# Optimization experiments

Hardware: AMD Instinct MI355X
Metric: run time of the kernel (lower is better)

Reference implementation:

```python
import jax, jax.numpy as jnp
import numpy as np

NUM_OPS = 8
NUM_CMP = 6
H = 2048
N = NUM_CMP + 2  # max number of anchors
NEG = -1e9


def setup_inputs() -> dict:
    key = jax.random.key(0)
    ks = jax.random.split(key, 8)
    s = 0.02
    return {
        "emb": jax.random.normal(ks[0], (NUM_OPS + 1, H), jnp.float32) * s,
        "w_ih": jax.random.normal(ks[1], (4 * H, H), jnp.float32) * s,
        "w_hh": jax.random.normal(ks[2], (4 * H, H), jnp.float32) * s,
        "b_ih": jnp.zeros((4 * H,), jnp.float32),
        "b_hh": jnp.zeros((4 * H,), jnp.float32),
        "w_opt": jax.random.normal(ks[3], (NUM_OPS, H), jnp.float32) * s,
        "b_opt": jnp.zeros((NUM_OPS,), jnp.float32),
        "w_attn1": jax.random.normal(ks[4], (H, H), jnp.float32) * s,
        "w_attn2": jax.random.normal(ks[5], (H, H), jnp.float32) * s,
        "v_attn": jax.random.normal(ks[6], (H,), jnp.float32) * s,
        "seed": 0,
    }


def _lstm(w_ih, w_hh, b_ih, b_hh, x, h, c):
    # torch LSTMCell, gate order i, f, g, o; x,h,c: [1,H]
    g = x @ w_ih.T + b_ih + h @ w_hh.T + b_hh
    i, f, gg, o = jnp.split(g, 4, axis=-1)
    c = jax.nn.sigmoid(f) * c + jax.nn.sigmoid(i) * jnp.tanh(gg)
    h = jax.nn.sigmoid(o) * jnp.tanh(c)
    return h, c


def _cat_stats(logits, idx):
    # cross_entropy(logits[None], idx) and detached entropy, logits: [K]
    logp = jax.nn.log_softmax(logits)
    lp = -logp[idx]
    logp_d = jax.lax.stop_gradient(logp)
    p = jnp.exp(logp_d)
    ent = -jnp.sum(jnp.where(p > 0, p * logp_d, 0.0))
    return lp, ent


def _generate_cell(params, hc, key):
    emb, w_ih, w_hh, b_ih, b_hh, w_opt, b_opt, w1, w2, v = params
    x = emb[0][None]  # [1,H]
    if hc is None:
        h = jnp.zeros((1, H), emb.dtype)
        c = jnp.zeros((1, H), emb.dtype)
    else:
        h, c = hc
    anchors = jnp.zeros((N, H), emb.dtype)
    anchors_w1 = jnp.zeros((N, H), emb.dtype)
    # two warmup steps; anchors stay zeros_like(h), anchors_w1 gets w1(h)
    for s in range(2):
        h, c = _lstm(w_ih, w_hh, b_ih, b_hh, x, h, c)
        anchors_w1 = anchors_w1.at[s].set((h @ w1.T)[0])

    def node_step(carry, inp):
        x, h, c, anchors, anchors_w1, ent, lp = carry
        s, k = inp
        mask = jnp.arange(N) < s
        idxs = []
        for i in range(2):
            h, c = _lstm(w_ih, w_hh, b_ih, b_hh, x, h, c)
            scores = jnp.tanh(h @ w2.T + anchors_w1) @ v  # [N]
            logits = jnp.where(mask, scores, NEG)
            idx = jax.random.categorical(jax.random.fold_in(k, i), logits)
            l, e = _cat_stats(logits, idx)
            lp = lp + l
            ent = ent + e
            x = anchors[idx][None]
            idxs.append(idx)
        ops = []
        for i in range(2):
            h, c = _lstm(w_ih, w_hh, b_ih, b_hh, x, h, c)
            logits = (h @ w_opt.T + b_opt)[0]  # [num_ops]
            op = jax.random.categorical(jax.random.fold_in(k, 2 + i), logits)
            l, e = _cat_stats(logits, op)
            lp = lp + l
            ent = ent + e
            x = emb[op + 1][None]
            ops.append(op)
        h, c = _lstm(w_ih, w_hh, b_ih, b_hh, x, h, c)
        anchors = anchors.at[s].set(h[0])
        anchors_w1 = anchors_w1.at[s].set((h @ w1.T)[0])
        x = emb[0][None]
        return (x, h, c, anchors, anchors_w1, ent, lp), (jnp.stack(idxs), jnp.stack(ops))

    zero = jnp.asarray(0.0, emb.dtype)
    carry0 = (x, h, c, anchors, anchors_w1, zero, zero)
    xs = (jnp.arange(2, N), jax.random.split(key, NUM_CMP))
    (x, h, c, _, _, ent, lp), (idx_seq, opt_seq) = jax.lax.scan(node_step, carry0, xs)
    return idx_seq, opt_seq, ent, lp, (h, c)


def reference(emb, w_ih, w_hh, b_ih, b_hh, w_opt, b_opt, w_attn1, w_attn2, v_attn, seed):
    params = (emb, w_ih, w_hh, b_ih, b_hh, w_opt, b_opt, w_attn1, w_attn2, v_attn)
    key = jax.random.key(seed)
    k1, k2 = jax.random.split(key)
    idx_n, opt_n, ent_n, lp_n, hc = _generate_cell(params, None, k1)
    idx_r, opt_r, ent_r, lp_r, _ = _generate_cell(params, hc, k2)
    return idx_n, opt_n, idx_r, opt_r, ent_n + ent_r, lp_n + lp_r
```

## Files before the change

kernel.cpp:

```cpp
#include <hip/hip_runtime.h>
#include <stdint.h>


#define HDIM 2048
#define NCAT 8
#define PARTITIONABLE 1

__device__ __forceinline__ unsigned rotl32(unsigned v, int r){ return (v<<r)|(v>>(32-r)); }

__device__ inline void tf_block(unsigned k0, unsigned k1, unsigned x0, unsigned x1,
                                unsigned& o0, unsigned& o1){
  unsigned ks0=k0, ks1=k1, ks2=0x1BD11BDAu ^ k0 ^ k1;
  const int ra[4]={13,15,26,6};
  const int rb[4]={17,29,16,24};
  x0 += ks0; x1 += ks1;
  #pragma unroll
  for (int i=0;i<4;++i){ x0+=x1; x1=rotl32(x1,ra[i]); x1^=x0; }
  x0+=ks1; x1+=ks2+1u;
  #pragma unroll
  for (int i=0;i<4;++i){ x0+=x1; x1=rotl32(x1,rb[i]); x1^=x0; }
  x0+=ks2; x1+=ks0+2u;
  #pragma unroll
  for (int i=0;i<4;++i){ x0+=x1; x1=rotl32(x1,ra[i]); x1^=x0; }
  x0+=ks0; x1+=ks1+3u;
  #pragma unroll
  for (int i=0;i<4;++i){ x0+=x1; x1=rotl32(x1,rb[i]); x1^=x0; }
  x0+=ks1; x1+=ks2+4u;
  #pragma unroll
  for (int i=0;i<4;++i){ x0+=x1; x1=rotl32(x1,ra[i]); x1^=x0; }
  x0+=ks2; x1+=ks0+5u;
  o0=x0; o1=x1;
}

__device__ __forceinline__ float sigm(float z){ return 1.0f/(1.0f+expf(-z)); }

__device__ inline int sample_and_stats(const float* logits, unsigned k0, unsigned k1,
                                       float* scal ){
  unsigned bits[NCAT];
#if PARTITIONABLE
  #pragma unroll
  for (int i=0;i<NCAT;++i){ unsigned a,b; tf_block(k0,k1,0u,(unsigned)i,a,b); bits[i]=a^b; }
#else
  #pragma unroll
  for (int i=0;i<4;++i){ unsigned a,b; tf_block(k0,k1,(unsigned)i,(unsigned)(i+4),a,b); bits[i]=a; bits[i+4]=b; }
#endif
  const float tiny = 1.1754943508222875e-38f;
  int best=0; float bv=-3.4e38f;
  #pragma unroll
  for (int j=0;j<NCAT;++j){
    float f = __uint_as_float((bits[j]>>9)|0x3f800000u) - 1.0f;
    float u = fmaxf(tiny, f*(1.0f-tiny)+tiny);
    float g = -logf(-logf(u));
    float vv = g + logits[j];
    if (vv > bv){ bv=vv; best=j; }
  }
  float m=-3.4e38f;
  #pragma unroll
  for (int j=0;j<NCAT;++j) m = fmaxf(m, logits[j]);
  float se=0.f;
  #pragma unroll
  for (int j=0;j<NCAT;++j) se += expf(logits[j]-m);
  float lse = logf(se);
  scal[1] += (m + lse - logits[best]);
  float ent = 0.f;
  #pragma unroll
  for (int j=0;j<NCAT;++j){
    float lpj = logits[j]-m-lse;
    float p = expf(lpj);
    if (p > 0.f) ent -= p*lpj;
  }
  scal[0] += ent;
  return best;
}


__global__ __launch_bounds__(256) void k_init(float* ws, const float* __restrict__ emb,
                                              const int* __restrict__ seedp, int cell){
  int t = threadIdx.x;
  float* anch = ws + 10240;
  float* aw1  = ws + 26624;
  for (int i=t;i<NCAT*HDIM;i+=256){ anch[i]=0.f; aw1[i]=0.f; }
  float* x = ws + 6144;
  for (int i=t;i<HDIM;i+=256){
    x[i] = emb[i];
    if (cell==0){ ws[i]=0.f; ws[4096+i]=0.f; }
  }
  if (t==0 && cell==0){
    float* scal = ws + 43008; scal[0]=0.f; scal[1]=0.f;
    unsigned* nk = (unsigned*)(ws + 43012);
    unsigned seed = (unsigned)seedp[0];
    unsigned K0=0u, K1=seed;
    unsigned ck[2][2];
#if PARTITIONABLE
    tf_block(K0,K1,0u,0u,ck[0][0],ck[0][1]);
    tf_block(K0,K1,0u,1u,ck[1][0],ck[1][1]);
    for (int cc=0;cc<2;++cc)
      for (int i=0;i<6;++i)
        tf_block(ck[cc][0],ck[cc][1],0u,(unsigned)i, nk[(cc*6+i)*2], nk[(cc*6+i)*2+1]);
#else
    unsigned a0,a1,b0,b1;
    tf_block(K0,K1,0u,2u,a0,a1);
    tf_block(K0,K1,1u,3u,b0,b1);
    ck[0][0]=a0; ck[0][1]=b0; ck[1][0]=a1; ck[1][1]=b1;
    for (int cc=0;cc<2;++cc){
      unsigned y0[6], y1[6];
      for (int i=0;i<6;++i) tf_block(ck[cc][0],ck[cc][1],(unsigned)i,(unsigned)(i+6),y0[i],y1[i]);
      unsigned flat[12];
      for (int i=0;i<6;++i){ flat[i]=y0[i]; flat[6+i]=y1[i]; }
      for (int i=0;i<6;++i){ nk[(cc*6+i)*2]=flat[2*i]; nk[(cc*6+i)*2+1]=flat[2*i+1]; }
    }
#endif
  }
}

__global__ __launch_bounds__(256) void k_lstm(
    const float* __restrict__ w_ih, const float* __restrict__ w_hh,
    const float* __restrict__ b_ih, const float* __restrict__ b_hh,
    const float* __restrict__ x, const float* __restrict__ h_in,
    float* __restrict__ h_out, float* __restrict__ c)
{
  int b  = blockIdx.x;
  int k0 = b*4;
  int wv = threadIdx.x >> 6;
  int ln = threadIdx.x & 63;
  __shared__ float gl[4][4];
  const float4* x4 = (const float4*)x;
  const float4* h4 = (const float4*)h_in;
  float acc[4];
  #pragma unroll
  for (int rr=0; rr<4; ++rr){
    int row = wv*HDIM + k0 + rr;
    const float4* wi = (const float4*)(w_ih + (size_t)row*HDIM);
    const float4* wh = (const float4*)(w_hh + (size_t)row*HDIM);
    float s = 0.f;
    #pragma unroll
    for (int it=0; it<8; ++it){
      int i4 = ln + it*64;
      float4 a = wi[i4]; float4 xv = x4[i4];
      float4 bb = wh[i4]; float4 hv = h4[i4];
      s += a.x*xv.x + a.y*xv.y + a.z*xv.z + a.w*xv.w;
      s += bb.x*hv.x + bb.y*hv.y + bb.z*hv.z + bb.w*hv.w;
    }
    acc[rr] = s;
  }
  #pragma unroll
  for (int rr=0; rr<4; ++rr){
    float s = acc[rr];
    #pragma unroll
    for (int m=32; m; m>>=1) s += __shfl_xor(s, m, 64);
    if (ln==0) gl[wv][rr] = s;
  }
  __syncthreads();
  if (threadIdx.x < 4){
    int kk = k0 + threadIdx.x;
    float gi = gl[0][threadIdx.x] + b_ih[kk]          + b_hh[kk];
    float gf = gl[1][threadIdx.x] + b_ih[HDIM+kk]     + b_hh[HDIM+kk];
    float gg = gl[2][threadIdx.x] + b_ih[2*HDIM+kk]   + b_hh[2*HDIM+kk];
    float go = gl[3][threadIdx.x] + b_ih[3*HDIM+kk]   + b_hh[3*HDIM+kk];
    float cn = sigm(gf)*c[kk] + sigm(gi)*tanhf(gg);
    c[kk] = cn;
    h_out[kk] = sigm(go)*tanhf(cn);
  }
}

__global__ __launch_bounds__(256) void k_matvec(const float* __restrict__ M,
    const float* __restrict__ vin, float* __restrict__ vout,
    const float* __restrict__ csrc, float* __restrict__ cdst,
    const float* __restrict__ xsrc, float* __restrict__ xdst)
{
  int b = blockIdx.x;
  int wv = threadIdx.x>>6, ln = threadIdx.x&63;
  const float4* v4 = (const float4*)vin;
  #pragma unroll
  for (int rr=0; rr<2; ++rr){
    int row = b*8 + wv*2 + rr;
    const float4* m4 = (const float4*)(M + (size_t)row*HDIM);
    float s=0.f;
    #pragma unroll
    for (int it=0; it<8; ++it){
      int i4 = ln + it*64;
      float4 a = m4[i4]; float4 v = v4[i4];
      s += a.x*v.x + a.y*v.y + a.z*v.z + a.w*v.w;
    }
    #pragma unroll
    for (int m=32; m; m>>=1) s += __shfl_xor(s, m, 64);
    if (ln==0) vout[row] = s;
  }
  int t = threadIdx.x;
  if (t < 8){
    int i = b*8 + t;
    if (cdst) cdst[i] = csrc[i];
    if (xdst) xdst[i] = xsrc[i];
  }
}

__global__ __launch_bounds__(512) void k_attn_sample(const float* __restrict__ t2,
    const float* __restrict__ aw1, const float* __restrict__ vatt,
    const float* __restrict__ anch, float* __restrict__ x, float* scal,
    const unsigned* __restrict__ nk, int cell, int node, int isub,
    float* __restrict__ outslot)
{
  __shared__ float sc[NCAT];
  __shared__ int sidx;
  int wv = threadIdx.x>>6, ln = threadIdx.x&63;
  const float* a = aw1 + (size_t)wv*HDIM;
  float s=0.f;
  for (int it=0; it<32; ++it){
    int d = ln + it*64;
    s += tanhf(t2[d] + a[d]) * vatt[d];
  }
  #pragma unroll
  for (int m=32; m; m>>=1) s += __shfl_xor(s, m, 64);
  if (ln==0) sc[wv]=s;
  __syncthreads();
  if (threadIdx.x==0){
    int svis = node + 2;
    float logits[NCAT];
    #pragma unroll
    for (int j=0;j<NCAT;++j) logits[j] = (j<svis)? sc[j] : -1e9f;
    unsigned f0,f1;
    tf_block(nk[(cell*6+node)*2], nk[(cell*6+node)*2+1], 0u, (unsigned)isub, f0, f1);
    int idx = sample_and_stats(logits, f0, f1, scal);
    *outslot = (float)idx;
    sidx = idx;
  }
  __syncthreads();
  const float* src = anch + (size_t)sidx*HDIM;
  for (int d=threadIdx.x; d<HDIM; d+=512) x[d]=src[d];
}

__global__ __launch_bounds__(512) void k_opt_sample(const float* __restrict__ h,
    const float* __restrict__ wopt, const float* __restrict__ bopt,
    const float* __restrict__ emb, float* __restrict__ x, float* scal,
    const unsigned* __restrict__ nk, int cell, int node, int isub,
    float* __restrict__ outslot)
{
  __shared__ float sc[NCAT];
  __shared__ int sop;
  int wv = threadIdx.x>>6, ln = threadIdx.x&63;
  const float4* m4 = (const float4*)(wopt + (size_t)wv*HDIM);
  const float4* h4 = (const float4*)h;
  float s=0.f;
  #pragma unroll
  for (int it=0; it<8; ++it){
    int i4 = ln + it*64;
    float4 a = m4[i4]; float4 v = h4[i4];
    s += a.x*v.x + a.y*v.y + a.z*v.z + a.w*v.w;
  }
  #pragma unroll
  for (int m=32; m; m>>=1) s += __shfl_xor(s, m, 64);
  if (ln==0) sc[wv] = s + bopt[wv];
  __syncthreads();
  if (threadIdx.x==0){
    float logits[NCAT];
    #pragma unroll
    for (int j=0;j<NCAT;++j) logits[j]=sc[j];
    unsigned f0,f1;
    tf_block(nk[(cell*6+node)*2], nk[(cell*6+node)*2+1], 0u, (unsigned)(2+isub), f0, f1);
    int op = sample_and_stats(logits, f0, f1, scal);
    *outslot = (float)op;
    sop = op;
  }
  __syncthreads();
  const float* src = emb + (size_t)(sop+1)*HDIM;
  for (int d=threadIdx.x; d<HDIM; d+=512) x[d]=src[d];
}

__global__ void k_fin(const float* __restrict__ scal, float* __restrict__ out){
  out[48] = scal[0];
  out[49] = scal[1];
}

extern "C" void kernel_launch(void* const* d_in, const int* in_sizes, int n_in,
                              void* d_out, int out_size, void* d_ws, size_t ws_size,
                              hipStream_t stream)
{
  (void)in_sizes; (void)n_in; (void)out_size; (void)ws_size;
  const float* emb   = (const float*)d_in[0];
  const float* w_ih  = (const float*)d_in[1];
  const float* w_hh  = (const float*)d_in[2];
  const float* b_ih  = (const float*)d_in[3];
  const float* b_hh  = (const float*)d_in[4];
  const float* w_opt = (const float*)d_in[5];
  const float* b_opt = (const float*)d_in[6];
  const float* w1    = (const float*)d_in[7];
  const float* w2    = (const float*)d_in[8];
  const float* vatt  = (const float*)d_in[9];
  const int*   seed  = (const int*)d_in[10];

  float* ws  = (float*)d_ws;
  float* out = (float*)d_out;

  float* h[2] = { ws+0, ws+2048 };
  float* c    = ws+4096;
  float* x    = ws+6144;
  float* t2   = ws+8192;
  float* anch = ws+10240;
  float* aw1  = ws+26624;
  float* scal = ws+43008;
  const unsigned* nk = (const unsigned*)(ws+43012);

  int cur = 0;
  for (int cell=0; cell<2; ++cell){
    k_init<<<1,256,0,stream>>>(ws, emb, seed, cell);
    for (int s=0; s<2; ++s){
      k_lstm<<<512,256,0,stream>>>(w_ih,w_hh,b_ih,b_hh,x,h[cur],h[cur^1],c); cur^=1;
      k_matvec<<<256,256,0,stream>>>(w1, h[cur], aw1 + s*HDIM,
                                     nullptr,nullptr,nullptr,nullptr);
    }
    for (int node=0; node<6; ++node){
      for (int i=0;i<2;++i){
        k_lstm<<<512,256,0,stream>>>(w_ih,w_hh,b_ih,b_hh,x,h[cur],h[cur^1],c); cur^=1;
        k_matvec<<<256,256,0,stream>>>(w2, h[cur], t2, nullptr,nullptr,nullptr,nullptr);
        k_attn_sample<<<1,512,0,stream>>>(t2, aw1, vatt, anch, x, scal, nk, cell, node, i,
                                          out + cell*24 + node*2 + i);
      }
      for (int i=0;i<2;++i){
        k_lstm<<<512,256,0,stream>>>(w_ih,w_hh,b_ih,b_hh,x,h[cur],h[cur^1],c); cur^=1;
        k_opt_sample<<<1,512,0,stream>>>(h[cur], w_opt, b_opt, emb, x, scal, nk, cell, node, i,
                                         out + cell*24 + 12 + node*2 + i);
      }
      k_lstm<<<512,256,0,stream>>>(w_ih,w_hh,b_ih,b_hh,x,h[cur],h[cur^1],c); cur^=1;
      k_matvec<<<256,256,0,stream>>>(w1, h[cur], aw1 + (node+2)*HDIM,
                                     h[cur], anch + (node+2)*HDIM, emb, x);
    }
  }
  k_fin<<<1,1,0,stream>>>(scal, out);
}
```

Before: 2.397 ms.

## Precompute embedding input gates, skip zero-input matvec, fuse sampling via last-block counters

Precomputes w_ih·emb[j]+bias for all nine embeddings so LSTM steps with embedding inputs skip the w_ih matvec, and skips it entirely when the input is a zero anchor. The input is tracked through a small control word rather than copied. Attention scoring and option sampling are folded into the preceding matvec kernels with an atomic last-block pattern, removing separate single-block launches. Each LSTM launch now runs more blocks with one row per block, at the cost of workspace for the gate table and atomic counters.

```diff
diff --git a/kernel.cpp b/kernel.cpp
--- a/kernel.cpp
+++ b/kernel.cpp
@@ -4,7 +4,22 @@
 
 #define HDIM 2048
 #define NCAT 8
+#define NROWS 8192
 #define PARTITIONABLE 1
+
+#define WS_H0    0
+#define WS_H1    2048
+#define WS_C     4096
+#define WS_X     6144
+#define WS_T2    8192
+#define WS_ANCH  10240
+#define WS_AW1   26624
+#define WS_SCAL  43008
+#define WS_XCTL  43010
+#define WS_NK    43012
+#define WS_CTR   43072
+#define WS_BIAS  43264
+#define WS_GIE   51456
 
 __device__ __forceinline__ unsigned rotl32(unsigned v, int r){ return (v<<r)|(v>>(32-r)); }
 
@@ -73,21 +88,53 @@
   return best;
 }
 
-
-__global__ __launch_bounds__(256) void k_init(float* ws, const float* __restrict__ emb,
-                                              const int* __restrict__ seedp, int cell){
+__global__ __launch_bounds__(256) void k_pre(const float* __restrict__ w_ih,
+    const float* __restrict__ b_ih, const float* __restrict__ b_hh,
+    const float* __restrict__ emb, float* __restrict__ gie, float* __restrict__ bias)
+{
+  int wv = threadIdx.x>>6, ln = threadIdx.x&63;
+  int r = blockIdx.x*4 + wv;
+  const float4* wr = (const float4*)(w_ih + (size_t)r*HDIM);
+  const float4* e4 = (const float4*)emb;
+  float acc[9];
+  #pragma unroll
+  for (int j=0;j<9;++j) acc[j]=0.f;
+  for (int it=0; it<8; ++it){
+    float4 a = wr[ln+it*64];
+    #pragma unroll
+    for (int j=0;j<9;++j){
+      float4 e = e4[j*512 + ln + it*64];
+      acc[j] += a.x*e.x + a.y*e.y + a.z*e.z + a.w*e.w;
+    }
+  }
+  #pragma unroll
+  for (int j=0;j<9;++j){
+    float s = acc[j];
+    #pragma unroll
+    for (int m=32;m;m>>=1) s += __shfl_xor(s,m,64);
+    acc[j]=s;
+  }
+  if (ln==0){
+    float b = b_ih[r] + b_hh[r];
+    bias[r] = b;
+    #pragma unroll
+    for (int j=0;j<9;++j) gie[(size_t)j*NROWS + r] = acc[j] + b;
+  }
+}
+
+__global__ __launch_bounds__(256) void k_init(float* ws, const int* __restrict__ seedp, int cell){
   int t = threadIdx.x;
-  float* anch = ws + 10240;
-  float* aw1  = ws + 26624;
+  float* anch = ws + WS_ANCH;
+  float* aw1  = ws + WS_AW1;
   for (int i=t;i<NCAT*HDIM;i+=256){ anch[i]=0.f; aw1[i]=0.f; }
-  float* x = ws + 6144;
-  for (int i=t;i<HDIM;i+=256){
-    x[i] = emb[i];
-    if (cell==0){ ws[i]=0.f; ws[4096+i]=0.f; }
-  }
+  if (cell==0){
+    for (int i=t;i<HDIM;i+=256){ ws[WS_H0+i]=0.f; ws[WS_C+i]=0.f; }
+    for (int i=t;i<64;i+=256) ((int*)(ws+WS_CTR))[i]=0;
+  }
+  if (t<2) ((int*)(ws+WS_XCTL))[t] = 0;
   if (t==0 && cell==0){
-    float* scal = ws + 43008; scal[0]=0.f; scal[1]=0.f;
-    unsigned* nk = (unsigned*)(ws + 43012);
+    ws[WS_SCAL]=0.f; ws[WS_SCAL+1]=0.f;
+    unsigned* nk = (unsigned*)(ws + WS_NK);
     unsigned seed = (unsigned)seedp[0];
     unsigned K0=0u, K1=seed;
     unsigned ck[2][2];
@@ -115,155 +162,185 @@
 
 __global__ __launch_bounds__(256) void k_lstm(
     const float* __restrict__ w_ih, const float* __restrict__ w_hh,
-    const float* __restrict__ b_ih, const float* __restrict__ b_hh,
-    const float* __restrict__ x, const float* __restrict__ h_in,
-    float* __restrict__ h_out, float* __restrict__ c)
+    const float* __restrict__ bias, const float* __restrict__ gie,
+    const int* __restrict__ xctl, const float* __restrict__ x,
+    const float* __restrict__ h_in, float* __restrict__ h_out, float* __restrict__ c,
+    int post, int* __restrict__ ctr,
+    const float* __restrict__ wopt, const float* __restrict__ bopt,
+    float* __restrict__ scal, const unsigned* __restrict__ nk,
+    int key_ofs, int isub, float* __restrict__ outslot, int* __restrict__ xctl_w)
 {
-  int b  = blockIdx.x;
-  int k0 = b*4;
+  int u  = blockIdx.x;
   int wv = threadIdx.x >> 6;
   int ln = threadIdx.x & 63;
-  __shared__ float gl[4][4];
-  const float4* x4 = (const float4*)x;
-  const float4* h4 = (const float4*)h_in;
-  float acc[4];
-  #pragma unroll
-  for (int rr=0; rr<4; ++rr){
-    int row = wv*HDIM + k0 + rr;
-    const float4* wi = (const float4*)(w_ih + (size_t)row*HDIM);
-    const float4* wh = (const float4*)(w_hh + (size_t)row*HDIM);
-    float s = 0.f;
+  int xmode = xctl[0], xidx = xctl[1];
+  size_t r = (size_t)wv*HDIM + u;
+
+  const float4* whr = (const float4*)(w_hh + r*HDIM);
+  const float4* h4  = (const float4*)h_in;
+  float s = 0.f;
+  #pragma unroll
+  for (int it=0; it<8; ++it){
+    float4 a = whr[ln+it*64]; float4 b = h4[ln+it*64];
+    s += a.x*b.x + a.y*b.y + a.z*b.z + a.w*b.w;
+  }
+  if (xmode==1){
+    const float4* wir = (const float4*)(w_ih + r*HDIM);
+    const float4* x4  = (const float4*)x;
     #pragma unroll
     for (int it=0; it<8; ++it){
-      int i4 = ln + it*64;
-      float4 a = wi[i4]; float4 xv = x4[i4];
-      float4 bb = wh[i4]; float4 hv = h4[i4];
-      s += a.x*xv.x + a.y*xv.y + a.z*xv.z + a.w*xv.w;
-      s += bb.x*hv.x + bb.y*hv.y + bb.z*hv.z + bb.w*hv.w;
-    }
-    acc[rr] = s;
-  }
-  #pragma unroll
-  for (int rr=0; rr<4; ++rr){
-    float s = acc[rr];
-    #pragma unroll
-    for (int m=32; m; m>>=1) s += __shfl_xor(s, m, 64);
-    if (ln==0) gl[wv][rr] = s;
-  }
-  __syncthreads();
-  if (threadIdx.x < 4){
-    int kk = k0 + threadIdx.x;
-    float gi = gl[0][threadIdx.x] + b_ih[kk]          + b_hh[kk];
-    float gf = gl[1][threadIdx.x] + b_ih[HDIM+kk]     + b_hh[HDIM+kk];
-    float gg = gl[2][threadIdx.x] + b_ih[2*HDIM+kk]   + b_hh[2*HDIM+kk];
-    float go = gl[3][threadIdx.x] + b_ih[3*HDIM+kk]   + b_hh[3*HDIM+kk];
-    float cn = sigm(gf)*c[kk] + sigm(gi)*tanhf(gg);
-    c[kk] = cn;
-    h_out[kk] = sigm(go)*tanhf(cn);
-  }
-}
-
-__global__ __launch_bounds__(256) void k_matvec(const float* __restrict__ M,
-    const float* __restrict__ vin, float* __restrict__ vout,
-    const float* __restrict__ csrc, float* __restrict__ cdst,
-    const float* __restrict__ xsrc, float* __restrict__ xdst)
+      float4 a = wir[ln+it*64]; float4 b = x4[ln+it*64];
+      s += a.x*b.x + a.y*b.y + a.z*b.z + a.w*b.w;
+    }
+  }
+  #pragma unroll
+  for (int m=32; m; m>>=1) s += __shfl_xor(s, m, 64);
+
+  __shared__ float gl[4];
+  __shared__ int slast;
+  __shared__ float sc[NCAT];
+  if (ln==0) gl[wv] = s;
+  __syncthreads();
+  if (threadIdx.x==0){
+    float a0,a1,a2,a3;
+    if (xmode==0){
+      const float* gc = gie + (size_t)xidx*NROWS;
+      a0=gc[u]; a1=gc[HDIM+u]; a2=gc[2*HDIM+u]; a3=gc[3*HDIM+u];
+    } else {
+      a0=bias[u]; a1=bias[HDIM+u]; a2=bias[2*HDIM+u]; a3=bias[3*HDIM+u];
+    }
+    float gi=gl[0]+a0, gf=gl[1]+a1, gg=gl[2]+a2, go=gl[3]+a3;
+    float cn = sigm(gf)*c[u] + sigm(gi)*tanhf(gg);
+    c[u] = cn;
+    h_out[u] = sigm(go)*tanhf(cn);
+    if (post){
+      __threadfence();
+      int old = atomicAdd(ctr, 1);
+      slast = (old == (int)gridDim.x - 1);
+    }
+  }
+  if (!post) return;
+  __syncthreads();
+  if (!slast) return;
+  __threadfence();
+  const float4* ho4 = (const float4*)h_out;
+  for (int j=wv; j<NCAT; j+=4){
+    const float4* wo = (const float4*)(wopt + (size_t)j*HDIM);
+    float t = 0.f;
+    #pragma unroll
+    for (int it=0; it<8; ++it){
+      float4 a = wo[ln+it*64]; float4 b = ho4[ln+it*64];
+      t += a.x*b.x + a.y*b.y + a.z*b.z + a.w*b.w;
+    }
+    #pragma unroll
+    for (int m=32; m; m>>=1) t += __shfl_xor(t, m, 64);
+    if (ln==0) sc[j] = t + bopt[j];
+  }
+  __syncthreads();
+  if (threadIdx.x==0){
+    float logits[NCAT];
+    #pragma unroll
+    for (int j=0;j<NCAT;++j) logits[j]=sc[j];
+    unsigned f0,f1;
+    tf_block(nk[key_ofs], nk[key_ofs+1], 0u, (unsigned)(2+isub), f0, f1);
+    int op = sample_and_stats(logits, f0, f1, scal);
+    *outslot = (float)op;
+    xctl_w[0] = 0; xctl_w[1] = op + 1;
+  }
+}
+
+__global__ __launch_bounds__(256) void k_w2attn(
+    const float* __restrict__ w2, const float* __restrict__ h,
+    float* __restrict__ t2, const float* __restrict__ aw1,
+    const float* __restrict__ vatt, const float* __restrict__ anch,
+    float* __restrict__ x, float* __restrict__ scal,
+    const unsigned* __restrict__ nk, int key_ofs, int isub, int svis,
+    int* __restrict__ ctr, int* __restrict__ xctl_w, float* __restrict__ outslot)
 {
-  int b = blockIdx.x;
   int wv = threadIdx.x>>6, ln = threadIdx.x&63;
-  const float4* v4 = (const float4*)vin;
-  #pragma unroll
-  for (int rr=0; rr<2; ++rr){
-    int row = b*8 + wv*2 + rr;
-    const float4* m4 = (const float4*)(M + (size_t)row*HDIM);
-    float s=0.f;
-    #pragma unroll
-    for (int it=0; it<8; ++it){
-      int i4 = ln + it*64;
-      float4 a = m4[i4]; float4 v = v4[i4];
-      s += a.x*v.x + a.y*v.y + a.z*v.z + a.w*v.w;
-    }
-    #pragma unroll
-    for (int m=32; m; m>>=1) s += __shfl_xor(s, m, 64);
-    if (ln==0) vout[row] = s;
-  }
-  int t = threadIdx.x;
-  if (t < 8){
-    int i = b*8 + t;
-    if (cdst) cdst[i] = csrc[i];
-    if (xdst) xdst[i] = xsrc[i];
-  }
-}
-
-__global__ __launch_bounds__(512) void k_attn_sample(const float* __restrict__ t2,
-    const float* __restrict__ aw1, const float* __restrict__ vatt,
-    const float* __restrict__ anch, float* __restrict__ x, float* scal,
-    const unsigned* __restrict__ nk, int cell, int node, int isub,
-    float* __restrict__ outslot)
-{
+  int r = blockIdx.x*4 + wv;
+  const float4* m4 = (const float4*)(w2 + (size_t)r*HDIM);
+  const float4* h4 = (const float4*)h;
+  float s = 0.f;
+  #pragma unroll
+  for (int it=0; it<8; ++it){
+    float4 a = m4[ln+it*64]; float4 b = h4[ln+it*64];
+    s += a.x*b.x + a.y*b.y + a.z*b.z + a.w*b.w;
+  }
+  #pragma unroll
+  for (int m=32; m; m>>=1) s += __shfl_xor(s, m, 64);
+  if (ln==0) t2[r] = s;
+
+  __shared__ int slast;
   __shared__ float sc[NCAT];
   __shared__ int sidx;
-  int wv = threadIdx.x>>6, ln = threadIdx.x&63;
-  const float* a = aw1 + (size_t)wv*HDIM;
-  float s=0.f;
-  for (int it=0; it<32; ++it){
-    int d = ln + it*64;
-    s += tanhf(t2[d] + a[d]) * vatt[d];
-  }
-  #pragma unroll
-  for (int m=32; m; m>>=1) s += __shfl_xor(s, m, 64);
-  if (ln==0) sc[wv]=s;
   __syncthreads();
   if (threadIdx.x==0){
-    int svis = node + 2;
+    __threadfence();
+    int old = atomicAdd(ctr, 1);
+    slast = (old == (int)gridDim.x - 1);
+  }
+  __syncthreads();
+  if (!slast) return;
+  __threadfence();
+  const float4* t24 = (const float4*)t2;
+  const float4* v4  = (const float4*)vatt;
+  for (int j=wv; j<NCAT; j+=4){
+    const float4* aj = (const float4*)(aw1 + (size_t)j*HDIM);
+    float t = 0.f;
+    for (int it=0; it<8; ++it){
+      float4 tt = t24[ln+it*64], aa = aj[ln+it*64], vv = v4[ln+it*64];
+      t += tanhf(tt.x+aa.x)*vv.x + tanhf(tt.y+aa.y)*vv.y
+         + tanhf(tt.z+aa.z)*vv.z + tanhf(tt.w+aa.w)*vv.w;
+    }
+    #pragma unroll
+    for (int m=32; m; m>>=1) t += __shfl_xor(t, m, 64);
+    if (ln==0) sc[j] = t;
+  }
+  __syncthreads();
+  if (threadIdx.x==0){
     float logits[NCAT];
     #pragma unroll
     for (int j=0;j<NCAT;++j) logits[j] = (j<svis)? sc[j] : -1e9f;
     unsigned f0,f1;
-    tf_block(nk[(cell*6+node)*2], nk[(cell*6+node)*2+1], 0u, (unsigned)isub, f0, f1);
+    tf_block(nk[key_ofs], nk[key_ofs+1], 0u, (unsigned)isub, f0, f1);
     int idx = sample_and_stats(logits, f0, f1, scal);
     *outslot = (float)idx;
     sidx = idx;
-  }
-  __syncthreads();
-  const float* src = anch + (size_t)sidx*HDIM;
-  for (int d=threadIdx.x; d<HDIM; d+=512) x[d]=src[d];
-}
-
-__global__ __launch_bounds__(512) void k_opt_sample(const float* __restrict__ h,
-    const float* __restrict__ wopt, const float* __restrict__ bopt,
-    const float* __restrict__ emb, float* __restrict__ x, float* scal,
-    const unsigned* __restrict__ nk, int cell, int node, int isub,
-    float* __restrict__ outslot)
+    xctl_w[0] = (idx < 2) ? 2 : 1;
+    xctl_w[1] = 0;
+  }
+  __syncthreads();
+  int si = sidx;
+  if (si >= 2){
+    const float4* src = (const float4*)(anch + (size_t)si*HDIM);
+    float4* dst = (float4*)x;
+    for (int i=threadIdx.x; i<512; i+=256) dst[i] = src[i];
+  }
+}
+
+__global__ __launch_bounds__(256) void k_w1post(const float* __restrict__ w1,
+    const float* __restrict__ h, float* __restrict__ aw1s,
+    float* __restrict__ anchs, int* __restrict__ xctl_w)
 {
-  __shared__ float sc[NCAT];
-  __shared__ int sop;
   int wv = threadIdx.x>>6, ln = threadIdx.x&63;
-  const float4* m4 = (const float4*)(wopt + (size_t)wv*HDIM);
+  int r = blockIdx.x*4 + wv;
+  const float4* m4 = (const float4*)(w1 + (size_t)r*HDIM);
   const float4* h4 = (const float4*)h;
-  float s=0.f;
+  float s = 0.f;
   #pragma unroll
   for (int it=0; it<8; ++it){
-    int i4 = ln + it*64;
-    float4 a = m4[i4]; float4 v = h4[i4];
-    s += a.x*v.x + a.y*v.y + a.z*v.z + a.w*v.w;
+    float4 a = m4[ln+it*64]; float4 b = h4[ln+it*64];
+    s += a.x*b.x + a.y*b.y + a.z*b.z + a.w*b.w;
   }
   #pragma unroll
   for (int m=32; m; m>>=1) s += __shfl_xor(s, m, 64);
-  if (ln==0) sc[wv] = s + bopt[wv];
-  __syncthreads();
-  if (threadIdx.x==0){
-    float logits[NCAT];
-    #pragma unroll
-    for (int j=0;j<NCAT;++j) logits[j]=sc[j];
-    unsigned f0,f1;
-    tf_block(nk[(cell*6+node)*2], nk[(cell*6+node)*2+1], 0u, (unsigned)(2+isub), f0, f1);
-    int op = sample_and_stats(logits, f0, f1, scal);
-    *outslot = (float)op;
-    sop = op;
-  }
-  __syncthreads();
-  const float* src = emb + (size_t)(sop+1)*HDIM;
-  for (int d=threadIdx.x; d<HDIM; d+=512) x[d]=src[d];
+  if (ln==0) aw1s[r] = s;
+  if (anchs && threadIdx.x<4){
+    int i = blockIdx.x*4 + threadIdx.x;
+    anchs[i] = h[i];
+  }
+  if (blockIdx.x==0 && threadIdx.x==0){ xctl_w[0]=0; xctl_w[1]=0; }
 }
 
 __global__ void k_fin(const float* __restrict__ scal, float* __restrict__ out){
@@ -291,38 +368,53 @@
   float* ws  = (float*)d_ws;
   float* out = (float*)d_out;
 
-  float* h[2] = { ws+0, ws+2048 };
-  float* c    = ws+4096;
-  float* x    = ws+6144;
-  float* t2   = ws+8192;
-  float* anch = ws+10240;
-  float* aw1  = ws+26624;
-  float* scal = ws+43008;
-  const unsigned* nk = (const unsigned*)(ws+43012);
-
-  int cur = 0;
+  float* h[2]  = { ws+WS_H0, ws+WS_H1 };
+  float* c     = ws+WS_C;
+  float* x     = ws+WS_X;
+  float* t2    = ws+WS_T2;
+  float* anch  = ws+WS_ANCH;
+  float* aw1   = ws+WS_AW1;
+  float* scal  = ws+WS_SCAL;
+  int*   xctl  = (int*)(ws+WS_XCTL);
+  const unsigned* nk = (const unsigned*)(ws+WS_NK);
+  int*   ctr   = (int*)(ws+WS_CTR);
+  float* bias  = ws+WS_BIAS;
+  float* gie   = ws+WS_GIE;
+
+  k_pre<<<2048,256,0,stream>>>(w_ih, b_ih, b_hh, emb, gie, bias);
+
+  int cur = 0, ctr_id = 0;
   for (int cell=0; cell<2; ++cell){
-    k_init<<<1,256,0,stream>>>(ws, emb, seed, cell);
+    k_init<<<1,256,0,stream>>>(ws, seed, cell);
     for (int s=0; s<2; ++s){
-      k_lstm<<<512,256,0,stream>>>(w_ih,w_hh,b_ih,b_hh,x,h[cur],h[cur^1],c); cur^=1;
-      k_matvec<<<256,256,0,stream>>>(w1, h[cur], aw1 + s*HDIM,
-                                     nullptr,nullptr,nullptr,nullptr);
+      k_lstm<<<2048,256,0,stream>>>(w_ih,w_hh,bias,gie,xctl,x,h[cur],h[cur^1],c,
+                                    0,nullptr,nullptr,nullptr,nullptr,nullptr,0,0,nullptr,nullptr);
+      cur^=1;
+      k_w1post<<<512,256,0,stream>>>(w1, h[cur], aw1 + s*HDIM, nullptr, xctl);
     }
     for (int node=0; node<6; ++node){
+      int key_ofs = (cell*6+node)*2;
       for (int i=0;i<2;++i){
-        k_lstm<<<512,256,0,stream>>>(w_ih,w_hh,b_ih,b_hh,x,h[cur],h[cur^1],c); cur^=1;
-        k_matvec<<<256,256,0,stream>>>(w2, h[cur], t2, nullptr,nullptr,nullptr,nullptr);
-        k_attn_sample<<<1,512,0,stream>>>(t2, aw1, vatt, anch, x, scal, nk, cell, node, i,
-                                          out + cell*24 + node*2 + i);
+        k_lstm<<<2048,256,0,stream>>>(w_ih,w_hh,bias,gie,xctl,x,h[cur],h[cur^1],c,
+                                      0,nullptr,nullptr,nullptr,nullptr,nullptr,0,0,nullptr,nullptr);
+        cur^=1;
+        k_w2attn<<<512,256,0,stream>>>(w2, h[cur], t2, aw1, vatt, anch, x, scal,
+                                       nk, key_ofs, i, node+2,
+                                       ctr + ctr_id, xctl, out + cell*24 + node*2 + i);
+        ctr_id++;
       }
       for (int i=0;i<2;++i){
-        k_lstm<<<512,256,0,stream>>>(w_ih,w_hh,b_ih,b_hh,x,h[cur],h[cur^1],c); cur^=1;
-        k_opt_sample<<<1,512,0,stream>>>(h[cur], w_opt, b_opt, emb, x, scal, nk, cell, node, i,
-                                         out + cell*24 + 12 + node*2 + i);
+        k_lstm<<<2048,256,0,stream>>>(w_ih,w_hh,bias,gie,xctl,x,h[cur],h[cur^1],c,
+                                      1, ctr + ctr_id, w_opt, b_opt, scal, nk,
+                                      key_ofs, i, out + cell*24 + 12 + node*2 + i, xctl);
+        ctr_id++;
+        cur^=1;
       }
-      k_lstm<<<512,256,0,stream>>>(w_ih,w_hh,b_ih,b_hh,x,h[cur],h[cur^1],c); cur^=1;
-      k_matvec<<<256,256,0,stream>>>(w1, h[cur], aw1 + (node+2)*HDIM,
-                                     h[cur], anch + (node+2)*HDIM, emb, x);
+      k_lstm<<<2048,256,0,stream>>>(w_ih,w_hh,bias,gie,xctl,x,h[cur],h[cur^1],c,
+                                    0,nullptr,nullptr,nullptr,nullptr,nullptr,0,0,nullptr,nullptr);
+      cur^=1;
+      k_w1post<<<512,256,0,stream>>>(w1, h[cur], aw1 + (node+2)*HDIM,
+                                     anch + (node+2)*HDIM, xctl);
     }
   }
   k_fin<<<1,1,0,stream>>>(scal, out);
```

New measurement: 3.294 ms. +37.4%, slower.
